# Kernel tuning notes

Hardware: AMD Instinct MI355X
Metric: run time of the kernel (lower is better)

The kernel has to match this reference:

```python
import jax, jax.numpy as jnp
import numpy as np

N_NODES = 100000
N_EDGES = 1600000


def gcn_conv(x, src, dst, W, b, n_nodes):
    # GCNConv: linear transform, then symmetrically-normalized scatter-add
    # (self-loops already appended to src/dst by caller)
    h = x @ W  # [N, out]
    ones = jnp.ones(src.shape[0], dtype=x.dtype)
    deg = jax.ops.segment_sum(ones, dst, num_segments=n_nodes)  # in-degree incl. self-loop
    dinv = jnp.where(deg > 0, jax.lax.rsqrt(deg), jnp.zeros_like(deg))
    norm = dinv[src] * dinv[dst]  # [E]
    out = jax.ops.segment_sum(norm[:, None] * h[src], dst, num_segments=n_nodes)
    return out + b


def setup_inputs() -> dict:
    key = jax.random.key(0)
    ks = jax.random.split(key, 8)
    in_ch, nhid, out_ch = 128, 48, 32
    x = jax.random.normal(ks[0], (N_NODES, in_ch), dtype=jnp.float32)
    edge_index = jax.random.randint(ks[1], (2, N_EDGES), 0, N_NODES, dtype=jnp.int64)
    s1 = 1.0 / np.sqrt(in_ch)
    s2 = 1.0 / np.sqrt(nhid)
    W1 = jax.random.uniform(ks[2], (in_ch, nhid), jnp.float32, -s1, s1)
    b1 = jnp.zeros((nhid,), jnp.float32)
    Wmu = jax.random.uniform(ks[3], (nhid, out_ch), jnp.float32, -s2, s2)
    bmu = jnp.zeros((out_ch,), jnp.float32)
    Wls = jax.random.uniform(ks[4], (nhid, out_ch), jnp.float32, -s2, s2)
    bls = jnp.zeros((out_ch,), jnp.float32)
    return {"x": x, "edge_index": edge_index, "W1": W1, "b1": b1,
            "Wmu": Wmu, "bmu": bmu, "Wls": Wls, "bls": bls}


def reference(x, edge_index, W1, b1, Wmu, bmu, Wls, bls):
    n = x.shape[0]
    loop = jnp.arange(n, dtype=edge_index.dtype)
    src = jnp.concatenate([edge_index[0], loop])
    dst = jnp.concatenate([edge_index[1], loop])
    h = jax.nn.relu(gcn_conv(x, src, dst, W1, b1, n))
    mu = gcn_conv(h, src, dst, Wmu, bmu, n)
    logstd = gcn_conv(h, src, dst, Wls, bls, n)
    return mu, logstd
```

## Files before the change

kernel.cpp:

```cpp
#include <hip/hip_runtime.h>
#include <hip/hip_fp16.h>

#define NN 100000
#define NE 1600000
#define FIN 128
#define FH 48
#define FO 32

#define LB 7
#define BKT_NODES 128
#define NBKT ((NN + BKT_NODES - 1) / BKT_NODES)
#define PBLK 250
#define EPB (NE / PBLK)
#define EPB4 (EPB / 4)
#define P2CAP 4096

#define GNPB 42
#define GCAP 1024

__device__ inline float2 h2f2(unsigned int u) {
  __half2 h = __builtin_bit_cast(__half2, u);
  return __half22float2(h);
}
__device__ inline unsigned int f2h2(float a, float b) {
  __half2 h = __floats2half2_rn(a, b);
  return __builtin_bit_cast(unsigned int, h);
}


__global__ __launch_bounds__(256) void p1_hist(const int4* __restrict__ dst4, int* __restrict__ H) {
  __shared__ int hist[NBKT];
  const int t = threadIdx.x, blk = blockIdx.x;
  for (int i = t; i < NBKT; i += 256) hist[i] = 0;
  __syncthreads();
  const int k0 = blk * EPB4;
  for (int k = t; k < EPB4; k += 256) {
    int4 d = dst4[k0 + k];
    atomicAdd(&hist[d.x >> LB], 1);
    atomicAdd(&hist[d.y >> LB], 1);
    atomicAdd(&hist[d.z >> LB], 1);
    atomicAdd(&hist[d.w >> LB], 1);
  }
  __syncthreads();
  for (int i = t; i < NBKT; i += 256) H[blk * NBKT + i] = hist[i];
}

__global__ __launch_bounds__(256) void p1_colscan(int* __restrict__ H, int* __restrict__ tot) {
  int b = blockIdx.x * 256 + threadIdx.x;
  if (b >= NBKT) return;
  int run = 0;
  for (int xcd = 0; xcd < 8; ++xcd) {
    for (int blk = xcd; blk < PBLK; blk += 8) {
      int v = H[blk * NBKT + b];
      H[blk * NBKT + b] = run;
      run += v;
    }
  }
  tot[b] = run;
}

__global__ __launch_bounds__(256) void p1_scan(const int* __restrict__ tot, int* __restrict__ base,
                                               int* __restrict__ off) {
  __shared__ int s[256];
  const int t = threadIdx.x;
  int c[4]; int sum = 0;
  #pragma unroll
  for (int k = 0; k < 4; ++k) {
    int idx = 4 * t + k;
    c[k] = (idx < NBKT) ? tot[idx] : 0;
    sum += c[k];
  }
  s[t] = sum;
  __syncthreads();
  for (int o = 1; o < 256; o <<= 1) {
    int v = (t >= o) ? s[t - o] : 0;
    __syncthreads();
    s[t] += v;
    __syncthreads();
  }
  int run = s[t] - sum;
  #pragma unroll
  for (int k = 0; k < 4; ++k) {
    int idx = 4 * t + k;
    if (idx < NBKT) base[idx] = run;
    run += c[k];
  }
  if (t == 255) { base[NBKT] = run; off[NN] = run; }
}

__global__ __launch_bounds__(256) void p1_scatter(const int4* __restrict__ src4, const int4* __restrict__ dst4,
                                                  const int* __restrict__ H, const int* __restrict__ base,
                                                  int* __restrict__ pairs) {
  __shared__ int cur[NBKT];
  const int t = threadIdx.x, blk = blockIdx.x;
  for (int i = t; i < NBKT; i += 256) cur[i] = base[i] + H[blk * NBKT + i];
  __syncthreads();
  const int k0 = blk * EPB4;
  for (int k = t; k < EPB4; k += 256) {
    int4 s = src4[k0 + k];
    int4 d = dst4[k0 + k];
    int b0 = d.x >> LB, b1 = d.y >> LB, b2 = d.z >> LB, b3 = d.w >> LB;
    int p0 = atomicAdd(&cur[b0], 1);
    pairs[p0] = s.x | ((d.x & (BKT_NODES - 1)) << 17);
    int p1 = atomicAdd(&cur[b1], 1);
    pairs[p1] = s.y | ((d.y & (BKT_NODES - 1)) << 17);
    int p2 = atomicAdd(&cur[b2], 1);
    pairs[p2] = s.z | ((d.z & (BKT_NODES - 1)) << 17);
    int p3 = atomicAdd(&cur[b3], 1);
    pairs[p3] = s.w | ((d.w & (BKT_NODES - 1)) << 17);
  }
}

__global__ __launch_bounds__(256) void p2_bucket(const int* __restrict__ pairs, const int* __restrict__ base,
                                                 int* __restrict__ csr, int* __restrict__ off,
                                                 float* __restrict__ dinv) {
  __shared__ int stage[P2CAP];
  __shared__ int cnt[BKT_NODES];
  __shared__ int s[BKT_NODES];
  const int t = threadIdx.x, b = blockIdx.x;
  const int j0 = base[b], j1 = base[b + 1];
  const int ne = j1 - j0;
  const bool fits = (ne <= P2CAP);

  if (t < BKT_NODES) cnt[t] = 0;
  if (fits) {
    for (int j = t; j < ne; j += 256) stage[j] = pairs[j0 + j];
  }
  __syncthreads();
  if (fits) {
    for (int j = t; j < ne; j += 256) atomicAdd(&cnt[stage[j] >> 17], 1);
  } else {
    for (int j = j0 + t; j < j1; j += 256) atomicAdd(&cnt[pairs[j] >> 17], 1);
  }
  __syncthreads();
  int myc = 0;
  if (t < BKT_NODES) { myc = cnt[t]; s[t] = myc; }
  __syncthreads();
  for (int o = 1; o < BKT_NODES; o <<= 1) {
    int v = (t >= o && t < BKT_NODES) ? s[t - o] : 0;
    __syncthreads();
    if (t < BKT_NODES) s[t] += v;
    __syncthreads();
  }
  int loc = 0;
  if (t < BKT_NODES) loc = s[t] - myc;
  const int n = b * BKT_NODES + t;
  if (t < BKT_NODES && n < NN) {
    off[n] = j0 + loc;
    dinv[n] = rsqrtf((float)myc + 1.0f);
  }
  __syncthreads();
  if (t < BKT_NODES) s[t] = loc;
  __syncthreads();
  if (fits) {
    for (int j = t; j < ne; j += 256) {
      int p = stage[j];
      int pos = atomicAdd(&s[p >> 17], 1);
      csr[j0 + pos] = p & 0x1FFFF;
    }
  } else {
    for (int j = j0 + t; j < j1; j += 256) {
      int p = pairs[j];
      int pos = atomicAdd(&s[p >> 17], 1);
      csr[j0 + pos] = p & 0x1FFFF;
    }
  }
}


__global__ __launch_bounds__(256) void k_gemm1(const float* __restrict__ x, const float* __restrict__ W1,
                                               const float* __restrict__ dinv, __half* __restrict__ t1h) {
  __shared__ float xs[64][132];
  __shared__ float ws[FIN][FH];
  const int t = threadIdx.x;
  const int row0 = blockIdx.x * 64;

  for (int i = t; i < FIN * FH; i += 256) ws[i / FH][i % FH] = W1[i];
  for (int i = t; i < 64 * (FIN / 4); i += 256) {
    int r = i >> 5, c4 = i & 31;
    float4 v = make_float4(0.f, 0.f, 0.f, 0.f);
    if (row0 + r < NN) v = ((const float4*)x)[(size_t)(row0 + r) * (FIN / 4) + c4];
    xs[r][c4 * 4 + 0] = v.x; xs[r][c4 * 4 + 1] = v.y;
    xs[r][c4 * 4 + 2] = v.z; xs[r][c4 * 4 + 3] = v.w;
  }
  __syncthreads();

  const int row = t >> 2;
  const int cg  = (t & 3) * 12;
  float acc[12];
  #pragma unroll
  for (int j = 0; j < 12; ++j) acc[j] = 0.f;

  #pragma unroll 4
  for (int k = 0; k < FIN; ++k) {
    float xv = xs[row][k];
    const float4* wp = (const float4*)&ws[k][cg];
    float4 w0 = wp[0], w1 = wp[1], w2 = wp[2];
    acc[0] += xv * w0.x; acc[1] += xv * w0.y; acc[2]  += xv * w0.z; acc[3]  += xv * w0.w;
    acc[4] += xv * w1.x; acc[5] += xv * w1.y; acc[6]  += xv * w1.z; acc[7]  += xv * w1.w;
    acc[8] += xv * w2.x; acc[9] += xv * w2.y; acc[10] += xv * w2.z; acc[11] += xv * w2.w;
  }

  const int grow = row0 + row;
  if (grow < NN) {
    const float dv = dinv[grow];
    #pragma unroll
    for (int j = 0; j < 12; ++j) acc[j] *= dv;
    uint2* p = (uint2*)(t1h + (size_t)grow * FH + cg);
    p[0] = make_uint2(f2h2(acc[0], acc[1]), f2h2(acc[2],  acc[3]));
    p[1] = make_uint2(f2h2(acc[4], acc[5]), f2h2(acc[6],  acc[7]));
    p[2] = make_uint2(f2h2(acc[8], acc[9]), f2h2(acc[10], acc[11]));
  }
}


#define ACC8(R)                                                                  \
  { float2 q0 = h2f2(R.x), q1 = h2f2(R.y), q2 = h2f2(R.z), q3 = h2f2(R.w);       \
    a[0] += q0.x; a[1] += q0.y; a[2] += q1.x; a[3] += q1.y;                      \
    a[4] += q2.x; a[5] += q2.y; a[6] += q3.x; a[7] += q3.y; }

#define GATHER_SUM(FEAT, SS)                                                     \
  {                                                                              \
    int j = jb;                                                                  \
    for (; j + 8 <= je; j += 8) {                                                \
      int s0 = SS[j],     s1 = SS[j + 1], s2 = SS[j + 2], s3 = SS[j + 3];        \
      int s4 = SS[j + 4], s5 = SS[j + 5], s6 = SS[j + 6], s7 = SS[j + 7];        \
      uint4 r0 = FEAT[(size_t)s0 * 6 + f8];                                      \
      uint4 r1 = FEAT[(size_t)s1 * 6 + f8];                                      \
      uint4 r2 = FEAT[(size_t)s2 * 6 + f8];                                      \
      uint4 r3 = FEAT[(size_t)s3 * 6 + f8];                                      \
      uint4 r4 = FEAT[(size_t)s4 * 6 + f8];                                      \
      uint4 r5 = FEAT[(size_t)s5 * 6 + f8];                                      \
      uint4 r6 = FEAT[(size_t)s6 * 6 + f8];                                      \
      uint4 r7 = FEAT[(size_t)s7 * 6 + f8];                                      \
      ACC8(r0) ACC8(r1) ACC8(r2) ACC8(r3) ACC8(r4) ACC8(r5) ACC8(r6) ACC8(r7)    \
    }                                                                            \
    for (; j + 4 <= je; j += 4) {                                                \
      int s0 = SS[j], s1 = SS[j + 1], s2 = SS[j + 2], s3 = SS[j + 3];            \
      uint4 r0 = FEAT[(size_t)s0 * 6 + f8];                                      \
      uint4 r1 = FEAT[(size_t)s1 * 6 + f8];                                      \
      uint4 r2 = FEAT[(size_t)s2 * 6 + f8];                                      \
      uint4 r3 = FEAT[(size_t)s3 * 6 + f8];                                      \
      ACC8(r0) ACC8(r1) ACC8(r2) ACC8(r3)                                        \
    }                                                                            \
    for (; j < je; ++j) {                                                        \
      int s = SS[j];                                                             \
      uint4 r = FEAT[(size_t)s * 6 + f8];                                        \
      ACC8(r)                                                                    \
    }                                                                            \
  }


__global__ __launch_bounds__(256) void k_gather1(const int* __restrict__ off, const int* __restrict__ csr,
                                                 const __half* __restrict__ feat16, const float* __restrict__ dinv,
                                                 const float* __restrict__ bias, __half* __restrict__ out16) {
  __shared__ int sstage[GCAP];
  const int t = threadIdx.x;
  const int n0 = blockIdx.x * GNPB;
  const int nend = (n0 + GNPB < NN) ? n0 + GNPB : NN;
  const int e0 = off[n0];
  const int ec = off[nend] - e0;
  const bool fits = (ec <= GCAP);
  if (fits) {
    for (int j = t; j < ec; j += 256) sstage[j] = csr[e0 + j];
  }
  __syncthreads();

  const int local = t / 6;
  const int f8 = t - local * 6;
  const int node = n0 + local;
  if (local >= GNPB || node >= NN) return;

  const uint4* feat = (const uint4*)feat16;
  const float di = dinv[node];
  uint4 rs = feat[(size_t)node * 6 + f8];
  float a[8];
  {
    float2 q0 = h2f2(rs.x), q1 = h2f2(rs.y), q2 = h2f2(rs.z), q3 = h2f2(rs.w);
    a[0] = q0.x; a[1] = q0.y; a[2] = q1.x; a[3] = q1.y;
    a[4] = q2.x; a[5] = q2.y; a[6] = q3.x; a[7] = q3.y;
  }

  if (fits) {
    const int jb = off[node] - e0;
    const int je = off[node + 1] - e0;
    GATHER_SUM(feat, sstage)
  } else {
    const int jb = off[node];
    const int je = off[node + 1];
    GATHER_SUM(feat, csr)
  }

  const float4* b4 = (const float4*)(bias + f8 * 8);
  float4 bb0 = b4[0], bb1 = b4[1];
  a[0] = di * fmaxf(di * a[0] + bb0.x, 0.f); a[1] = di * fmaxf(di * a[1] + bb0.y, 0.f);
  a[2] = di * fmaxf(di * a[2] + bb0.z, 0.f); a[3] = di * fmaxf(di * a[3] + bb0.w, 0.f);
  a[4] = di * fmaxf(di * a[4] + bb1.x, 0.f); a[5] = di * fmaxf(di * a[5] + bb1.y, 0.f);
  a[6] = di * fmaxf(di * a[6] + bb1.z, 0.f); a[7] = di * fmaxf(di * a[7] + bb1.w, 0.f);
  uint4 o;
  o.x = f2h2(a[0], a[1]); o.y = f2h2(a[2], a[3]);
  o.z = f2h2(a[4], a[5]); o.w = f2h2(a[6], a[7]);
  ((uint4*)out16)[(size_t)node * 6 + f8] = o;
}


__global__ __launch_bounds__(256) void k_gather_gemm2(const int* __restrict__ off, const int* __restrict__ csr,
                                                      const __half* __restrict__ feat16, const float* __restrict__ dinv,
                                                      const float* __restrict__ Wmu, const float* __restrict__ bmu,
                                                      const float* __restrict__ Wls, const float* __restrict__ bls,
                                                      float* __restrict__ out) {
  __shared__ int   sstage[GCAP];
  __shared__ float wall[FH][2 * FO];
  __shared__ float as2[GNPB][FH + 4];
  const int t = threadIdx.x;
  const int n0 = blockIdx.x * GNPB;
  const int nend = (n0 + GNPB < NN) ? n0 + GNPB : NN;
  const int e0 = off[n0];
  const int ec = off[nend] - e0;
  const bool fits = (ec <= GCAP);

  for (int i = t; i < FH * 2 * FO; i += 256) {
    int k = i >> 6, c = i & 63;
    wall[k][c] = (c < FO) ? Wmu[k * FO + c] : Wls[k * FO + (c - FO)];
  }
  if (fits) {
    for (int j = t; j < ec; j += 256) sstage[j] = csr[e0 + j];
  }
  __syncthreads();

  const int local = t / 6;
  const int f8 = t - local * 6;
  const int node = n0 + local;
  const bool active = (local < GNPB) && (node < NN);

  if (active) {
    const uint4* feat = (const uint4*)feat16;
    const float di = dinv[node];
    uint4 rs = feat[(size_t)node * 6 + f8];
    float a[8];
    {
      float2 q0 = h2f2(rs.x), q1 = h2f2(rs.y), q2 = h2f2(rs.z), q3 = h2f2(rs.w);
      a[0] = q0.x; a[1] = q0.y; a[2] = q1.x; a[3] = q1.y;
      a[4] = q2.x; a[5] = q2.y; a[6] = q3.x; a[7] = q3.y;
    }
    if (fits) {
      const int jb = off[node] - e0;
      const int je = off[node + 1] - e0;
      GATHER_SUM(feat, sstage)
    } else {
      const int jb = off[node];
      const int je = off[node + 1];
      GATHER_SUM(feat, csr)
    }
    float* ap = &as2[local][f8 * 8];
    ap[0] = di * a[0]; ap[1] = di * a[1]; ap[2] = di * a[2]; ap[3] = di * a[3];
    ap[4] = di * a[4]; ap[5] = di * a[5]; ap[6] = di * a[6]; ap[7] = di * a[7];
  }
  __syncthreads();

  for (int o = t; o < GNPB * 2 * FO; o += 256) {
    const int ln = o >> 6;
    const int c = o & 63;
    const int grow = n0 + ln;
    if (grow < NN) {
      float acc = (c < FO) ? bmu[c] : bls[c - FO];
      #pragma unroll
      for (int k = 0; k < FH; ++k) acc += as2[ln][k] * wall[k][c];
      if (c < FO) out[(size_t)grow * FO + c] = acc;
      else        out[(size_t)NN * FO + (size_t)grow * FO + (c - FO)] = acc;
    }
  }
}


extern "C" void kernel_launch(void* const* d_in, const int* in_sizes, int n_in,
                              void* d_out, int out_size, void* d_ws, size_t ws_size,
                              hipStream_t stream) {
  const float* x   = (const float*)d_in[0];
  const int*   ei  = (const int*)d_in[1];
  const float* W1  = (const float*)d_in[2];
  const float* b1  = (const float*)d_in[3];
  const float* Wmu = (const float*)d_in[4];
  const float* bmu = (const float*)d_in[5];
  const float* Wls = (const float*)d_in[6];
  const float* bls = (const float*)d_in[7];
  float* out = (float*)d_out;

  const int4* src4 = (const int4*)ei;
  const int4* dst4 = (const int4*)(ei + NE);

  char* base_p = (char*)d_ws;
  int*    pairs = (int*)base_p;
  int*    csr   = pairs + (size_t)NE;
  __half* t1h   = (__half*)(csr + (size_t)NE);
  __half* h16   = t1h + (size_t)NN * FH;
  int*    H     = (int*)(h16 + (size_t)NN * FH);
  int*    tot   = H + (size_t)PBLK * NBKT;
  int*    bkb   = tot + NBKT;
  int*    off   = bkb + NBKT + 1;
  float*  dinv  = (float*)(off + NN + 1);

  p1_hist   <<<PBLK, 256, 0, stream>>>(dst4, H);
  p1_colscan<<<(NBKT + 255) / 256, 256, 0, stream>>>(H, tot);
  p1_scan   <<<1, 256, 0, stream>>>(tot, bkb, off);
  p1_scatter<<<PBLK, 256, 0, stream>>>(src4, dst4, H, bkb, pairs);
  p2_bucket <<<NBKT, 256, 0, stream>>>(pairs, bkb, csr, off, dinv);

  k_gemm1<<<(NN + 63) / 64, 256, 0, stream>>>(x, W1, dinv, t1h);
  k_gather1<<<(NN + GNPB - 1) / GNPB, 256, 0, stream>>>(off, csr, t1h, dinv, b1, h16);

  k_gather_gemm2<<<(NN + GNPB - 1) / GNPB, 256, 0, stream>>>(
      off, csr, h16, dinv, Wmu, bmu, Wls, bls, out);
}
```

Measured before the change: 274.5 us.

## Split gather and dense GEMM in layer two, drop LDS CSR staging

Removes the shared-memory staging of CSR indices and the block barrier from both gather kernels, and adds occupancy hints to them. The second layer's fused gather and GEMM is split into a pure gather kernel that writes fp32 aggregates to a new workspace buffer, followed by a separate register-tiled dense kernel. The goal is higher occupancy and less LDS and barrier cost in the latency-bound gathers. In exchange it adds an extra round trip of about 19 MB through global memory and one more kernel launch.

```diff
diff --git a/kernel.cpp b/kernel.cpp
--- a/kernel.cpp
+++ b/kernel.cpp
@@ -16,7 +16,6 @@
 #define P2CAP 4096
 
 #define GNPB 42
-#define GCAP 1024
 
 __device__ inline float2 h2f2(unsigned int u) {
   __half2 h = __builtin_bit_cast(__half2, u);
@@ -251,28 +250,16 @@
   }
 
 
-__global__ __launch_bounds__(256) void k_gather1(const int* __restrict__ off, const int* __restrict__ csr,
-                                                 const __half* __restrict__ feat16, const float* __restrict__ dinv,
-                                                 const float* __restrict__ bias, __half* __restrict__ out16) {
-  __shared__ int sstage[GCAP];
+__global__ __launch_bounds__(256, 6) void k_gather1(const int* __restrict__ off, const int* __restrict__ csr,
+                                                    const __half* __restrict__ feat16, const float* __restrict__ dinv,
+                                                    const float* __restrict__ bias, __half* __restrict__ out16) {
   const int t = threadIdx.x;
-  const int n0 = blockIdx.x * GNPB;
-  const int nend = (n0 + GNPB < NN) ? n0 + GNPB : NN;
-  const int e0 = off[n0];
-  const int ec = off[nend] - e0;
-  const bool fits = (ec <= GCAP);
-  if (fits) {
-    for (int j = t; j < ec; j += 256) sstage[j] = csr[e0 + j];
-  }
-  __syncthreads();
-
   const int local = t / 6;
   const int f8 = t - local * 6;
-  const int node = n0 + local;
+  const int node = blockIdx.x * GNPB + local;
   if (local >= GNPB || node >= NN) return;
 
   const uint4* feat = (const uint4*)feat16;
-  const float di = dinv[node];
   uint4 rs = feat[(size_t)node * 6 + f8];
   float a[8];
   {
@@ -281,16 +268,11 @@
     a[4] = q2.x; a[5] = q2.y; a[6] = q3.x; a[7] = q3.y;
   }
 
-  if (fits) {
-    const int jb = off[node] - e0;
-    const int je = off[node + 1] - e0;
-    GATHER_SUM(feat, sstage)
-  } else {
-    const int jb = off[node];
-    const int je = off[node + 1];
-    GATHER_SUM(feat, csr)
-  }
-
+  const int jb = off[node];
+  const int je = off[node + 1];
+  GATHER_SUM(feat, csr)
+
+  const float di = dinv[node];
   const float4* b4 = (const float4*)(bias + f8 * 8);
   float4 bb0 = b4[0], bb1 = b4[1];
   a[0] = di * fmaxf(di * a[0] + bb0.x, 0.f); a[1] = di * fmaxf(di * a[1] + bb0.y, 0.f);
@@ -304,71 +286,80 @@
 }
 
 
-__global__ __launch_bounds__(256) void k_gather_gemm2(const int* __restrict__ off, const int* __restrict__ csr,
-                                                      const __half* __restrict__ feat16, const float* __restrict__ dinv,
-                                                      const float* __restrict__ Wmu, const float* __restrict__ bmu,
-                                                      const float* __restrict__ Wls, const float* __restrict__ bls,
-                                                      float* __restrict__ out) {
-  __shared__ int   sstage[GCAP];
+__global__ __launch_bounds__(256, 6) void k_gather2(const int* __restrict__ off, const int* __restrict__ csr,
+                                                    const __half* __restrict__ feat16, const float* __restrict__ dinv,
+                                                    float* __restrict__ aggf) {
+  const int t = threadIdx.x;
+  const int local = t / 6;
+  const int f8 = t - local * 6;
+  const int node = blockIdx.x * GNPB + local;
+  if (local >= GNPB || node >= NN) return;
+
+  const uint4* feat = (const uint4*)feat16;
+  uint4 rs = feat[(size_t)node * 6 + f8];
+  float a[8];
+  {
+    float2 q0 = h2f2(rs.x), q1 = h2f2(rs.y), q2 = h2f2(rs.z), q3 = h2f2(rs.w);
+    a[0] = q0.x; a[1] = q0.y; a[2] = q1.x; a[3] = q1.y;
+    a[4] = q2.x; a[5] = q2.y; a[6] = q3.x; a[7] = q3.y;
+  }
+
+  const int jb = off[node];
+  const int je = off[node + 1];
+  GATHER_SUM(feat, csr)
+
+  const float di = dinv[node];
+  float4* ap = (float4*)(aggf + (size_t)node * FH + f8 * 8);
+  ap[0] = make_float4(di * a[0], di * a[1], di * a[2], di * a[3]);
+  ap[1] = make_float4(di * a[4], di * a[5], di * a[6], di * a[7]);
+}
+
+
+__global__ __launch_bounds__(256) void k_dense(const float* __restrict__ aggf,
+                                               const float* __restrict__ Wmu, const float* __restrict__ bmu,
+                                               const float* __restrict__ Wls, const float* __restrict__ bls,
+                                               float* __restrict__ out) {
   __shared__ float wall[FH][2 * FO];
-  __shared__ float as2[GNPB][FH + 4];
+  __shared__ float as[64][FH + 1];
   const int t = threadIdx.x;
-  const int n0 = blockIdx.x * GNPB;
-  const int nend = (n0 + GNPB < NN) ? n0 + GNPB : NN;
-  const int e0 = off[n0];
-  const int ec = off[nend] - e0;
-  const bool fits = (ec <= GCAP);
+  const int n0 = blockIdx.x * 64;
 
   for (int i = t; i < FH * 2 * FO; i += 256) {
     int k = i >> 6, c = i & 63;
     wall[k][c] = (c < FO) ? Wmu[k * FO + c] : Wls[k * FO + (c - FO)];
   }
-  if (fits) {
-    for (int j = t; j < ec; j += 256) sstage[j] = csr[e0 + j];
-  }
-  __syncthreads();
-
-  const int local = t / 6;
-  const int f8 = t - local * 6;
-  const int node = n0 + local;
-  const bool active = (local < GNPB) && (node < NN);
-
-  if (active) {
-    const uint4* feat = (const uint4*)feat16;
-    const float di = dinv[node];
-    uint4 rs = feat[(size_t)node * 6 + f8];
-    float a[8];
-    {
-      float2 q0 = h2f2(rs.x), q1 = h2f2(rs.y), q2 = h2f2(rs.z), q3 = h2f2(rs.w);
-      a[0] = q0.x; a[1] = q0.y; a[2] = q1.x; a[3] = q1.y;
-      a[4] = q2.x; a[5] = q2.y; a[6] = q3.x; a[7] = q3.y;
-    }
-    if (fits) {
-      const int jb = off[node] - e0;
-      const int je = off[node + 1] - e0;
-      GATHER_SUM(feat, sstage)
-    } else {
-      const int jb = off[node];
-      const int je = off[node + 1];
-      GATHER_SUM(feat, csr)
-    }
-    float* ap = &as2[local][f8 * 8];
-    ap[0] = di * a[0]; ap[1] = di * a[1]; ap[2] = di * a[2]; ap[3] = di * a[3];
-    ap[4] = di * a[4]; ap[5] = di * a[5]; ap[6] = di * a[6]; ap[7] = di * a[7];
-  }
-  __syncthreads();
-
-  for (int o = t; o < GNPB * 2 * FO; o += 256) {
-    const int ln = o >> 6;
-    const int c = o & 63;
-    const int grow = n0 + ln;
-    if (grow < NN) {
-      float acc = (c < FO) ? bmu[c] : bls[c - FO];
-      #pragma unroll
-      for (int k = 0; k < FH; ++k) acc += as2[ln][k] * wall[k][c];
-      if (c < FO) out[(size_t)grow * FO + c] = acc;
-      else        out[(size_t)NN * FO + (size_t)grow * FO + (c - FO)] = acc;
-    }
+  for (int i = t; i < 64 * FH; i += 256) {
+    int r = i / FH, c = i - r * FH;
+    as[r][c] = (n0 + r < NN) ? aggf[(size_t)(n0 + r) * FH + c] : 0.f;
+  }
+  __syncthreads();
+
+  const int ln = t >> 2;
+  const int cb = (t & 3) * 16;
+  float acc[16];
+  #pragma unroll
+  for (int j = 0; j < 16; ++j) acc[j] = (cb + j < FO) ? bmu[cb + j] : bls[cb + j - FO];
+
+  #pragma unroll 4
+  for (int k = 0; k < FH; ++k) {
+    float av = as[ln][k];
+    const float4* wp = (const float4*)&wall[k][cb];
+    float4 w0 = wp[0], w1 = wp[1], w2 = wp[2], w3 = wp[3];
+    acc[0]  += av * w0.x; acc[1]  += av * w0.y; acc[2]  += av * w0.z; acc[3]  += av * w0.w;
+    acc[4]  += av * w1.x; acc[5]  += av * w1.y; acc[6]  += av * w1.z; acc[7]  += av * w1.w;
+    acc[8]  += av * w2.x; acc[9]  += av * w2.y; acc[10] += av * w2.z; acc[11] += av * w2.w;
+    acc[12] += av * w3.x; acc[13] += av * w3.y; acc[14] += av * w3.z; acc[15] += av * w3.w;
+  }
+
+  const int grow = n0 + ln;
+  if (grow < NN) {
+    float4* po;
+    if (cb < FO) po = (float4*)(out + (size_t)grow * FO + cb);
+    else         po = (float4*)(out + (size_t)NN * FO + (size_t)grow * FO + (cb - FO));
+    po[0] = make_float4(acc[0],  acc[1],  acc[2],  acc[3]);
+    po[1] = make_float4(acc[4],  acc[5],  acc[6],  acc[7]);
+    po[2] = make_float4(acc[8],  acc[9],  acc[10], acc[11]);
+    po[3] = make_float4(acc[12], acc[13], acc[14], acc[15]);
   }
 }
 
@@ -394,7 +385,8 @@
   int*    csr   = pairs + (size_t)NE;
   __half* t1h   = (__half*)(csr + (size_t)NE);
   __half* h16   = t1h + (size_t)NN * FH;
-  int*    H     = (int*)(h16 + (size_t)NN * FH);
+  float*  aggf  = (float*)(h16 + (size_t)NN * FH);
+  int*    H     = (int*)(aggf + (size_t)NN * FH);
   int*    tot   = H + (size_t)PBLK * NBKT;
   int*    bkb   = tot + NBKT;
   int*    off   = bkb + NBKT + 1;
@@ -409,6 +401,6 @@
   k_gemm1<<<(NN + 63) / 64, 256, 0, stream>>>(x, W1, dinv, t1h);
   k_gather1<<<(NN + GNPB - 1) / GNPB, 256, 0, stream>>>(off, csr, t1h, dinv, b1, h16);
 
-  k_gather_gemm2<<<(NN + GNPB - 1) / GNPB, 256, 0, stream>>>(
-      off, csr, h16, dinv, Wmu, bmu, Wls, bls, out);
-}
+  k_gather2<<<(NN + GNPB - 1) / GNPB, 256, 0, stream>>>(off, csr, h16, dinv, aggf);
+  k_dense<<<(NN + 63) / 64, 256, 0, stream>>>(aggf, Wmu, bmu, Wls, bls, out);
+}
```

After: 283.9 us. 3.4% more time.

## Compute one row per thread in gemm1 and drop shared CSR staging in gathers

Applied to the files above, without the earlier changes.

The first GEMM now gives each thread a whole output row with 48 accumulators. Each thread streams its own x row straight from global memory instead of staging a 64-row tile in shared memory, and writes the result as full 16-byte half vectors. Both gather kernels stop copying the block's CSR slice into shared memory and read neighbour indices directly from global memory, which removes the staging loop and a barrier. The dinv load moves after the gather, and gather1 gets an occupancy hint in its launch bounds. The risks are uncoalesced, strided x reads across the threads of a wavefront, higher register pressure from the 48 accumulators, and global-memory latency on the index reads.

```diff
diff --git a/kernel.cpp b/kernel.cpp
--- a/kernel.cpp
+++ b/kernel.cpp
@@ -16,7 +16,6 @@
 #define P2CAP 4096
 
 #define GNPB 42
-#define GCAP 1024
 
 __device__ inline float2 h2f2(unsigned int u) {
   __half2 h = __builtin_bit_cast(__half2, u);
@@ -170,46 +169,48 @@
 
 __global__ __launch_bounds__(256) void k_gemm1(const float* __restrict__ x, const float* __restrict__ W1,
                                                const float* __restrict__ dinv, __half* __restrict__ t1h) {
-  __shared__ float xs[64][132];
-  __shared__ float ws[FIN][FH];
+  __shared__ float ws[FIN * FH];
   const int t = threadIdx.x;
-  const int row0 = blockIdx.x * 64;
-
-  for (int i = t; i < FIN * FH; i += 256) ws[i / FH][i % FH] = W1[i];
-  for (int i = t; i < 64 * (FIN / 4); i += 256) {
-    int r = i >> 5, c4 = i & 31;
-    float4 v = make_float4(0.f, 0.f, 0.f, 0.f);
-    if (row0 + r < NN) v = ((const float4*)x)[(size_t)(row0 + r) * (FIN / 4) + c4];
-    xs[r][c4 * 4 + 0] = v.x; xs[r][c4 * 4 + 1] = v.y;
-    xs[r][c4 * 4 + 2] = v.z; xs[r][c4 * 4 + 3] = v.w;
-  }
-  __syncthreads();
-
-  const int row = t >> 2;
-  const int cg  = (t & 3) * 12;
-  float acc[12];
+  for (int i = t; i < FIN * FH / 4; i += 256) ((float4*)ws)[i] = ((const float4*)W1)[i];
+  __syncthreads();
+
+  const int row = blockIdx.x * 256 + t;
+  if (row >= NN) return;
+
+  float acc[48];
   #pragma unroll
-  for (int j = 0; j < 12; ++j) acc[j] = 0.f;
-
-  #pragma unroll 4
-  for (int k = 0; k < FIN; ++k) {
-    float xv = xs[row][k];
-    const float4* wp = (const float4*)&ws[k][cg];
-    float4 w0 = wp[0], w1 = wp[1], w2 = wp[2];
-    acc[0] += xv * w0.x; acc[1] += xv * w0.y; acc[2]  += xv * w0.z; acc[3]  += xv * w0.w;
-    acc[4] += xv * w1.x; acc[5] += xv * w1.y; acc[6]  += xv * w1.z; acc[7]  += xv * w1.w;
-    acc[8] += xv * w2.x; acc[9] += xv * w2.y; acc[10] += xv * w2.z; acc[11] += xv * w2.w;
-  }
-
-  const int grow = row0 + row;
-  if (grow < NN) {
-    const float dv = dinv[grow];
+  for (int j = 0; j < 48; ++j) acc[j] = 0.f;
+
+  const float4* xr = (const float4*)(x + (size_t)row * FIN);
+  #pragma unroll 1
+  for (int kk = 0; kk < FIN / 4; ++kk) {
+    float4 xv = xr[kk];
+    const float* wk = ws + (kk * 4) * FH;
     #pragma unroll
-    for (int j = 0; j < 12; ++j) acc[j] *= dv;
-    uint2* p = (uint2*)(t1h + (size_t)grow * FH + cg);
-    p[0] = make_uint2(f2h2(acc[0], acc[1]), f2h2(acc[2],  acc[3]));
-    p[1] = make_uint2(f2h2(acc[4], acc[5]), f2h2(acc[6],  acc[7]));
-    p[2] = make_uint2(f2h2(acc[8], acc[9]), f2h2(acc[10], acc[11]));
+    for (int e = 0; e < 4; ++e) {
+      const float xs_ = (e == 0) ? xv.x : (e == 1) ? xv.y : (e == 2) ? xv.z : xv.w;
+      const float4* w4 = (const float4*)(wk + e * FH);
+      #pragma unroll
+      for (int c4 = 0; c4 < 12; ++c4) {
+        float4 w = w4[c4];
+        acc[c4 * 4 + 0] += xs_ * w.x;
+        acc[c4 * 4 + 1] += xs_ * w.y;
+        acc[c4 * 4 + 2] += xs_ * w.z;
+        acc[c4 * 4 + 3] += xs_ * w.w;
+      }
+    }
+  }
+
+  const float dv = dinv[row];
+  uint4* po = (uint4*)(t1h + (size_t)row * FH);
+  #pragma unroll
+  for (int g = 0; g < 6; ++g) {
+    uint4 o;
+    o.x = f2h2(acc[g * 8 + 0] * dv, acc[g * 8 + 1] * dv);
+    o.y = f2h2(acc[g * 8 + 2] * dv, acc[g * 8 + 3] * dv);
+    o.z = f2h2(acc[g * 8 + 4] * dv, acc[g * 8 + 5] * dv);
+    o.w = f2h2(acc[g * 8 + 6] * dv, acc[g * 8 + 7] * dv);
+    po[g] = o;
   }
 }
 
@@ -251,28 +252,16 @@
   }
 
 
-__global__ __launch_bounds__(256) void k_gather1(const int* __restrict__ off, const int* __restrict__ csr,
-                                                 const __half* __restrict__ feat16, const float* __restrict__ dinv,
-                                                 const float* __restrict__ bias, __half* __restrict__ out16) {
-  __shared__ int sstage[GCAP];
+__global__ __launch_bounds__(256, 6) void k_gather1(const int* __restrict__ off, const int* __restrict__ csr,
+                                                    const __half* __restrict__ feat16, const float* __restrict__ dinv,
+                                                    const float* __restrict__ bias, __half* __restrict__ out16) {
   const int t = threadIdx.x;
-  const int n0 = blockIdx.x * GNPB;
-  const int nend = (n0 + GNPB < NN) ? n0 + GNPB : NN;
-  const int e0 = off[n0];
-  const int ec = off[nend] - e0;
-  const bool fits = (ec <= GCAP);
-  if (fits) {
-    for (int j = t; j < ec; j += 256) sstage[j] = csr[e0 + j];
-  }
-  __syncthreads();
-
   const int local = t / 6;
   const int f8 = t - local * 6;
-  const int node = n0 + local;
+  const int node = blockIdx.x * GNPB + local;
   if (local >= GNPB || node >= NN) return;
 
   const uint4* feat = (const uint4*)feat16;
-  const float di = dinv[node];
   uint4 rs = feat[(size_t)node * 6 + f8];
   float a[8];
   {
@@ -281,16 +270,11 @@
     a[4] = q2.x; a[5] = q2.y; a[6] = q3.x; a[7] = q3.y;
   }
 
-  if (fits) {
-    const int jb = off[node] - e0;
-    const int je = off[node + 1] - e0;
-    GATHER_SUM(feat, sstage)
-  } else {
-    const int jb = off[node];
-    const int je = off[node + 1];
-    GATHER_SUM(feat, csr)
-  }
-
+  const int jb = off[node];
+  const int je = off[node + 1];
+  GATHER_SUM(feat, csr)
+
+  const float di = dinv[node];
   const float4* b4 = (const float4*)(bias + f8 * 8);
   float4 bb0 = b4[0], bb1 = b4[1];
   a[0] = di * fmaxf(di * a[0] + bb0.x, 0.f); a[1] = di * fmaxf(di * a[1] + bb0.y, 0.f);
@@ -309,24 +293,15 @@
                                                       const float* __restrict__ Wmu, const float* __restrict__ bmu,
                                                       const float* __restrict__ Wls, const float* __restrict__ bls,
                                                       float* __restrict__ out) {
-  __shared__ int   sstage[GCAP];
   __shared__ float wall[FH][2 * FO];
   __shared__ float as2[GNPB][FH + 4];
   const int t = threadIdx.x;
   const int n0 = blockIdx.x * GNPB;
-  const int nend = (n0 + GNPB < NN) ? n0 + GNPB : NN;
-  const int e0 = off[n0];
-  const int ec = off[nend] - e0;
-  const bool fits = (ec <= GCAP);
 
   for (int i = t; i < FH * 2 * FO; i += 256) {
     int k = i >> 6, c = i & 63;
     wall[k][c] = (c < FO) ? Wmu[k * FO + c] : Wls[k * FO + (c - FO)];
   }
-  if (fits) {
-    for (int j = t; j < ec; j += 256) sstage[j] = csr[e0 + j];
-  }
-  __syncthreads();
 
   const int local = t / 6;
   const int f8 = t - local * 6;
@@ -335,7 +310,6 @@
 
   if (active) {
     const uint4* feat = (const uint4*)feat16;
-    const float di = dinv[node];
     uint4 rs = feat[(size_t)node * 6 + f8];
     float a[8];
     {
@@ -343,15 +317,11 @@
       a[0] = q0.x; a[1] = q0.y; a[2] = q1.x; a[3] = q1.y;
       a[4] = q2.x; a[5] = q2.y; a[6] = q3.x; a[7] = q3.y;
     }
-    if (fits) {
-      const int jb = off[node] - e0;
-      const int je = off[node + 1] - e0;
-      GATHER_SUM(feat, sstage)
-    } else {
-      const int jb = off[node];
-      const int je = off[node + 1];
-      GATHER_SUM(feat, csr)
-    }
+    const int jb = off[node];
+    const int je = off[node + 1];
+    GATHER_SUM(feat, csr)
+
+    const float di = dinv[node];
     float* ap = &as2[local][f8 * 8];
     ap[0] = di * a[0]; ap[1] = di * a[1]; ap[2] = di * a[2]; ap[3] = di * a[3];
     ap[4] = di * a[4]; ap[5] = di * a[5]; ap[6] = di * a[6]; ap[7] = di * a[7];
@@ -406,7 +376,7 @@
   p1_scatter<<<PBLK, 256, 0, stream>>>(src4, dst4, H, bkb, pairs);
   p2_bucket <<<NBKT, 256, 0, stream>>>(pairs, bkb, csr, off, dinv);
 
-  k_gemm1<<<(NN + 63) / 64, 256, 0, stream>>>(x, W1, dinv, t1h);
+  k_gemm1<<<(NN + 255) / 256, 256, 0, stream>>>(x, W1, dinv, t1h);
   k_gather1<<<(NN + GNPB - 1) / GNPB, 256, 0, stream>>>(off, csr, t1h, dinv, b1, h16);
 
   k_gather_gemm2<<<(NN + GNPB - 1) / GNPB, 256, 0, stream>>>(
```

New measurement: 272.2 us. Within noise of the previous version (-0.8%).
